# Kernel optimization log

Hardware: AMD Instinct MI355X
Metric: run time of the kernel (lower is better)

The kernel has to match this reference:

```python
import jax, jax.numpy as jnp
import numpy as np

N = 4096
IN_DIM = 128
OUT_DIM = 64
LEAKY_SLOPE = 0.2


def setup_inputs() -> dict:
    key = jax.random.key(0)
    ks = jax.random.split(key, 8)
    H = jax.random.normal(ks[0], (N, IN_DIM), dtype=jnp.float32)
    # dense 0/1 adjacency per relation (int constants w.r.t. autodiff)
    A_buys = jax.random.randint(ks[1], (N, N), 0, 2, dtype=jnp.int32)
    A_views = jax.random.randint(ks[2], (N, N), 0, 2, dtype=jnp.int32)
    # xavier_uniform for W (stored [in, out]; Wh = H @ W == torch Linear with weight W.T)
    s_w = float(np.sqrt(6.0 / (IN_DIM + OUT_DIM)))
    W_buys = jax.random.uniform(ks[3], (IN_DIM, OUT_DIM), jnp.float32, -s_w, s_w)
    W_views = jax.random.uniform(ks[4], (IN_DIM, OUT_DIM), jnp.float32, -s_w, s_w)
    # xavier_uniform on a.view(1, 2*out_dim)
    s_a = float(np.sqrt(6.0 / (1 + 2 * OUT_DIM)))
    a_buys = jax.random.uniform(ks[5], (2 * OUT_DIM,), jnp.float32, -s_a, s_a)
    a_views = jax.random.uniform(ks[6], (2 * OUT_DIM,), jnp.float32, -s_a, s_a)
    bias = jnp.zeros((OUT_DIM,), dtype=jnp.float32)
    return {"H": H, "A_buys": A_buys, "A_views": A_views,
            "W_buys": W_buys, "W_views": W_views,
            "a_buys": a_buys, "a_views": a_views, "bias": bias}


def _relation(H, A, W, a):
    Wh = H @ W                                  # [N, OUT]
    # (cat(Wh_i, Wh_j) * a).sum(-1) == Wh_i @ a[:OUT] + Wh_j @ a[OUT:]
    s_i = Wh @ a[:OUT_DIM]                      # [N]
    s_j = Wh @ a[OUT_DIM:]                      # [N]
    e = jax.nn.leaky_relu(s_i[:, None] + s_j[None, :], LEAKY_SLOPE)  # [N, N]
    e = jnp.where(A == 0, -jnp.inf, e)
    alpha = jnp.nan_to_num(jax.nn.softmax(e, axis=1))                # isolated rows -> 0
    return alpha @ Wh                           # [N, OUT]


def reference(H, A_buys, A_views, W_buys, W_views, a_buys, a_views, bias):
    agg = _relation(H, A_buys, W_buys, a_buys) + _relation(H, A_views, W_views, a_views)
    return agg + bias
```

## Files before the change

### kernel.cpp

```cpp
#include <hip/hip_runtime.h>

#define NN 4096
#define IND 128
#define OUTD 64
#define WJ 128
#define NWIN 8
#define LOG2E 1.44269504088896340736f

typedef __attribute__((ext_vector_type(4))) float  floatx4;
typedef __attribute__((ext_vector_type(8))) __bf16 bf16x8;
typedef __attribute__((ext_vector_type(4))) int    intx4;

#if __has_builtin(__builtin_amdgcn_exp2f)
#define EXP2(x) __builtin_amdgcn_exp2f(x)
#else
#define EXP2(x) exp2f(x)
#endif

__device__ __forceinline__ unsigned short f2bf(float f) {
  unsigned int u = __float_as_uint(f);
  u += 0x7fffu + ((u >> 16) & 1u);
  return (unsigned short)(u >> 16);
}

__global__ __launch_bounds__(256) void gat_prep(
    const float* __restrict__ H,
    const float* __restrict__ W0, const float* __restrict__ W1,
    const float* __restrict__ av0, const float* __restrict__ av1,
    unsigned short* __restrict__ whF,
    float* __restrict__ sA, float* __restrict__ sB)
{
  const int rel = blockIdx.y;
  const float* __restrict__ W  = rel ? W1 : W0;
  const float* __restrict__ av = rel ? av1 : av0;
  const int i0 = blockIdx.x * 16;
  const int t = threadIdx.x;
  const int c = t & 63;
  const int wv = __builtin_amdgcn_readfirstlane(t >> 6);
  const float* __restrict__ hp = H + (size_t)(i0 + wv * 4) * IND;

  float acc0 = 0.f, acc1 = 0.f, acc2 = 0.f, acc3 = 0.f;
#pragma unroll 8
  for (int k = 0; k < IND; k += 4) {
    float4 h0 = *(const float4*)(hp + k);
    float4 h1 = *(const float4*)(hp + IND + k);
    float4 h2 = *(const float4*)(hp + 2 * IND + k);
    float4 h3 = *(const float4*)(hp + 3 * IND + k);
    float w0 = W[(k + 0) * OUTD + c];
    float w1 = W[(k + 1) * OUTD + c];
    float w2 = W[(k + 2) * OUTD + c];
    float w3 = W[(k + 3) * OUTD + c];
    acc0 += h0.x * w0 + h0.y * w1 + h0.z * w2 + h0.w * w3;
    acc1 += h1.x * w0 + h1.y * w1 + h1.z * w2 + h1.w * w3;
    acc2 += h2.x * w0 + h2.y * w1 + h2.z * w2 + h2.w * w3;
    acc3 += h3.x * w0 + h3.y * w1 + h3.z * w2 + h3.w * w3;
  }

  const float alo = av[c] * LOG2E, ahi = av[OUTD + c] * LOG2E;
  float pa0 = acc0 * alo, pa1 = acc1 * alo, pa2 = acc2 * alo, pa3 = acc3 * alo;
  float pb0 = acc0 * ahi, pb1 = acc1 * ahi, pb2 = acc2 * ahi, pb3 = acc3 * ahi;
#pragma unroll
  for (int off = 32; off >= 1; off >>= 1) {
    pa0 += __shfl_xor(pa0, off); pa1 += __shfl_xor(pa1, off);
    pa2 += __shfl_xor(pa2, off); pa3 += __shfl_xor(pa3, off);
    pb0 += __shfl_xor(pb0, off); pb1 += __shfl_xor(pb1, off);
    pb2 += __shfl_xor(pb2, off); pb3 += __shfl_xor(pb3, off);
  }
  const int ibase = i0 + wv * 4;
  if (c == 0) {
    float* sa = sA + rel * NN + ibase;
    float* sb = sB + rel * NN + ibase;
    sa[0] = pa0; sa[1] = pa1; sa[2] = pa2; sa[3] = pa3;
    sb[0] = pb0; sb[1] = pb1; sb[2] = pb2; sb[3] = pb3;
  }

  unsigned long long packed =
      (unsigned long long)f2bf(acc0)        | ((unsigned long long)f2bf(acc1) << 16) |
      ((unsigned long long)f2bf(acc2) << 32) | ((unsigned long long)f2bf(acc3) << 48);
  *(unsigned long long*)(whF + ((size_t)(rel * 512 + (ibase >> 3)) * 64 + c) * 8 + (ibase & 7)) = packed;
}

__global__ __launch_bounds__(256, 2) void gat_fused(
    const int* __restrict__ A0, const int* __restrict__ A1,
    const unsigned short* __restrict__ whF,
    const float* __restrict__ sA, const float* __restrict__ sB,
    float* __restrict__ numer,
    float* __restrict__ denom)
{
  __shared__ char lds[4][2][4096];
  const int rel  = blockIdx.y;
  const int i0   = blockIdx.x * 16;
  const int t    = threadIdx.x;
  const int w    = t >> 6;
  const int lane = t & 63;
  const int quad = lane >> 4;
  const int m    = lane & 15;
  const int lj   = lane & 31;
  const int half = lane >> 5;
  const int s_st = lj >> 1;
  const int wboff = s_st * 256 + (lj & 1) * 8;
  const int* __restrict__ A = rel ? A1 : A0;
  const unsigned short* __restrict__ wh = whF + (size_t)rel * 512 * 64 * 8;
  const float* __restrict__ sbp = sB + rel * NN;

  float si_r[8];
#pragma unroll
  for (int p = 0; p < 8; p++) si_r[p] = sA[rel * NN + i0 + 2 * p + half];

  const int jbase = w * (NWIN * WJ);

  floatx4 acc0 = {0.f,0.f,0.f,0.f}, acc1 = acc0, acc2 = acc0, acc3 = acc0, acc4 = acc0;
  bf16x8 vone;
#pragma unroll
  for (int k = 0; k < 8; k++) vone[k] = (__bf16)1.0f;

  intx4  av2[2][8];
  float4 sjv2[2];
  bf16x8 b[4][4];

  auto issueA = [&](int win) {
    const int jw = jbase + win * WJ;
    const int buf = win & 1;
    sjv2[buf] = *(const float4*)(sbp + jw + lj * 4);
    const int* pA = A + (size_t)(i0 + half) * NN + jw + lj * 4;
#pragma unroll
    for (int p = 0; p < 8; p++)
      av2[buf][p] = __builtin_nontemporal_load((const intx4*)(pA + (size_t)(2 * p) * NN));
  };

  auto stage = [&](int win) {
    const int buf = win & 1;
    char* slice = lds[w][buf];
    const float4 sjv = sjv2[buf];
#pragma unroll
    for (int p = 0; p < 8; p++) {
      const int rp = 2 * p + half;
      const float si = si_r[p];
      float t0 = si + sjv.x, t1 = si + sjv.y, t2 = si + sjv.z, t3 = si + sjv.w;
      float e0 = EXP2(fmaxf(t0, 0.2f * t0));
      float e1 = EXP2(fmaxf(t1, 0.2f * t1));
      float e2 = EXP2(fmaxf(t2, 0.2f * t2));
      float e3 = EXP2(fmaxf(t3, 0.2f * t3));
      const intx4 a4 = av2[buf][p];
      e0 = a4[0] ? e0 : 0.f;
      e1 = a4[1] ? e1 : 0.f;
      e2 = a4[2] ? e2 : 0.f;
      e3 = a4[3] ? e3 : 0.f;
      uint2 pk;
      pk.x = (unsigned)f2bf(e0) | ((unsigned)f2bf(e1) << 16);
      pk.y = (unsigned)f2bf(e2) | ((unsigned)f2bf(e3) << 16);
      *(uint2*)(slice + wboff + ((rp ^ s_st) & 15) * 16) = pk;
    }
  };

  auto issueB = [&](int win) {
    const int jw = jbase + win * WJ;
    const unsigned short* bb = wh + ((size_t)(jw >> 3) + quad) * 512 + (size_t)m * 8;
#pragma unroll
    for (int ks = 0; ks < 4; ks++)
#pragma unroll
      for (int nt = 0; nt < 4; nt++)
        b[ks][nt] = *(const bf16x8*)(bb + (size_t)ks * 2048 + nt * 128);
  };

  auto domfma = [&](int win) {
    char* slice = lds[w][win & 1];
    bf16x8 afr[4];
#pragma unroll
    for (int ks = 0; ks < 4; ks++) {
      const int s = ks * 4 + quad;
      afr[ks] = *(const bf16x8*)(slice + s * 256 + ((m ^ s) & 15) * 16);
    }
#pragma unroll
    for (int ks = 0; ks < 4; ks++) {
      acc0 = __builtin_amdgcn_mfma_f32_16x16x32_bf16(afr[ks], b[ks][0], acc0, 0, 0, 0);
      acc1 = __builtin_amdgcn_mfma_f32_16x16x32_bf16(afr[ks], b[ks][1], acc1, 0, 0, 0);
      acc2 = __builtin_amdgcn_mfma_f32_16x16x32_bf16(afr[ks], b[ks][2], acc2, 0, 0, 0);
      acc3 = __builtin_amdgcn_mfma_f32_16x16x32_bf16(afr[ks], b[ks][3], acc3, 0, 0, 0);
      acc4 = __builtin_amdgcn_mfma_f32_16x16x32_bf16(afr[ks], vone,     acc4, 0, 0, 0);
    }
  };

  issueA(0);
  stage(0);
  issueA(1);

#pragma unroll
  for (int win = 0; win < NWIN; win++) {
    issueB(win);
    if (win + 2 < NWIN) issueA(win + 2);
    if (win + 1 < NWIN) stage(win + 1);
    domfma(win);
  }

  float* redw  = (float*)lds[w][0];
  float* dredw = (float*)lds[w][1];
#pragma unroll
  for (int r = 0; r < 4; r++) {
    const int row = quad * 4 + r;
    redw[row * 64 + 0 * 16 + m] = acc0[r];
    redw[row * 64 + 1 * 16 + m] = acc1[r];
    redw[row * 64 + 2 * 16 + m] = acc2[r];
    redw[row * 64 + 3 * 16 + m] = acc3[r];
  }
  if (m == 0) {
#pragma unroll
    for (int r = 0; r < 4; r++) dredw[quad * 4 + r] = acc4[r];
  }
  __syncthreads();

  const int c  = t & 63;
  const int r0 = t >> 6;
  const size_t base = (size_t)rel * NN;
#pragma unroll
  for (int rr = r0; rr < 16; rr += 4) {
    float nsum = 0.f, ds = 0.f;
#pragma unroll
    for (int ww = 0; ww < 4; ww++) {
      nsum += ((const float*)lds[ww][0])[rr * 64 + c];
      ds   += ((const float*)lds[ww][1])[rr];
    }
    numer[(base + i0 + rr) * OUTD + c] = nsum;
    if (c == 0) denom[base + i0 + rr] = ds;
  }
}

__global__ __launch_bounds__(256) void gat_combine(
    const float* __restrict__ numer, const float* __restrict__ denom,
    const float* __restrict__ bias, float* __restrict__ out)
{
  const int idx = blockIdx.x * 256 + threadIdx.x;
  const int i  = idx >> 4;
  const int c4 = idx & 15;
  const float4* nv = (const float4*)numer;

  float4 o = ((const float4*)bias)[c4];
#pragma unroll
  for (int rel = 0; rel < 2; rel++) {
    const size_t base = (size_t)rel * NN + i;
    float4 n = nv[base * 16 + c4];
    float  d = denom[base];
    float inv = d > 0.f ? 1.f / d : 0.f;
    o.x += n.x * inv; o.y += n.y * inv; o.z += n.z * inv; o.w += n.w * inv;
  }
  ((float4*)out)[idx] = o;
}

extern "C" void kernel_launch(void* const* d_in, const int* in_sizes, int n_in,
                              void* d_out, int out_size, void* d_ws, size_t ws_size,
                              hipStream_t stream) {
  const float* H    = (const float*)d_in[0];
  const int*   A0   = (const int*)d_in[1];
  const int*   A1   = (const int*)d_in[2];
  const float* W0   = (const float*)d_in[3];
  const float* W1   = (const float*)d_in[4];
  const float* av0  = (const float*)d_in[5];
  const float* av1  = (const float*)d_in[6];
  const float* bias = (const float*)d_in[7];
  float* out = (float*)d_out;

  const size_t whF_b = (size_t)2 * 512 * 64 * 8 * 2;
  const size_t s_b   = (size_t)2 * NN * 4;

  unsigned short* whF   = (unsigned short*)d_ws;
  float*          sA    = (float*)((char*)d_ws + whF_b);
  float*          sB    = (float*)((char*)d_ws + whF_b + s_b);
  float*          numer = (float*)((char*)d_ws + whF_b + 2 * s_b);
  float*          denom = numer + (size_t)2 * NN * OUTD;

  gat_prep<<<dim3(NN / 16, 2), 256, 0, stream>>>(H, W0, W1, av0, av1, whF, sA, sB);
  gat_fused<<<dim3(NN / 16, 2), 256, 0, stream>>>(A0, A1, whF, sA, sB, numer, denom);
  gat_combine<<<(NN * OUTD / 4) / 256, 256, 0, stream>>>(numer, denom, bias, out);
}
```

Before: 180.8 us.

## Fuse both relations into one block and fold the combine kernel into the epilogue

```diff
diff --git a/kernel.cpp b/kernel.cpp
--- a/kernel.cpp
+++ b/kernel.cpp
@@ -80,18 +80,18 @@
   *(unsigned long long*)(whF + ((size_t)(rel * 512 + (ibase >> 3)) * 64 + c) * 8 + (ibase & 7)) = packed;
 }
 
-__global__ __launch_bounds__(256, 2) void gat_fused(
+__global__ __launch_bounds__(512, 2) void gat_fused(
     const int* __restrict__ A0, const int* __restrict__ A1,
     const unsigned short* __restrict__ whF,
     const float* __restrict__ sA, const float* __restrict__ sB,
-    float* __restrict__ numer,
-    float* __restrict__ denom)
+    const float* __restrict__ bias,
+    float* __restrict__ out)
 {
-  __shared__ char lds[4][2][4096];
-  const int rel  = blockIdx.y;
+  __shared__ char lds[8][2][4096];
   const int i0   = blockIdx.x * 16;
   const int t    = threadIdx.x;
   const int w    = t >> 6;
+  const int rel  = w >> 2;
   const int lane = t & 63;
   const int quad = lane >> 4;
   const int m    = lane & 15;
@@ -107,7 +107,7 @@
 #pragma unroll
   for (int p = 0; p < 8; p++) si_r[p] = sA[rel * NN + i0 + 2 * p + half];
 
-  const int jbase = w * (NWIN * WJ);
+  const int jbase = (w & 3) * (NWIN * WJ);
 
   floatx4 acc0 = {0.f,0.f,0.f,0.f}, acc1 = acc0, acc2 = acc0, acc3 = acc0, acc4 = acc0;
   bf16x8 vone;
@@ -211,39 +211,21 @@
 
   const int c  = t & 63;
   const int r0 = t >> 6;
-  const size_t base = (size_t)rel * NN;
-#pragma unroll
-  for (int rr = r0; rr < 16; rr += 4) {
-    float nsum = 0.f, ds = 0.f;
+  const float bc = bias[c];
+#pragma unroll
+  for (int rr = r0; rr < 16; rr += 8) {
+    float n0 = 0.f, n1 = 0.f, d0 = 0.f, d1 = 0.f;
 #pragma unroll
     for (int ww = 0; ww < 4; ww++) {
-      nsum += ((const float*)lds[ww][0])[rr * 64 + c];
-      ds   += ((const float*)lds[ww][1])[rr];
-    }
-    numer[(base + i0 + rr) * OUTD + c] = nsum;
-    if (c == 0) denom[base + i0 + rr] = ds;
-  }
-}
-
-__global__ __launch_bounds__(256) void gat_combine(
-    const float* __restrict__ numer, const float* __restrict__ denom,
-    const float* __restrict__ bias, float* __restrict__ out)
-{
-  const int idx = blockIdx.x * 256 + threadIdx.x;
-  const int i  = idx >> 4;
-  const int c4 = idx & 15;
-  const float4* nv = (const float4*)numer;
-
-  float4 o = ((const float4*)bias)[c4];
-#pragma unroll
-  for (int rel = 0; rel < 2; rel++) {
-    const size_t base = (size_t)rel * NN + i;
-    float4 n = nv[base * 16 + c4];
-    float  d = denom[base];
-    float inv = d > 0.f ? 1.f / d : 0.f;
-    o.x += n.x * inv; o.y += n.y * inv; o.z += n.z * inv; o.w += n.w * inv;
-  }
-  ((float4*)out)[idx] = o;
+      n0 += ((const float*)lds[ww][0])[rr * 64 + c];
+      d0 += ((const float*)lds[ww][1])[rr];
+      n1 += ((const float*)lds[ww + 4][0])[rr * 64 + c];
+      d1 += ((const float*)lds[ww + 4][1])[rr];
+    }
+    const float inv0 = d0 > 0.f ? 1.f / d0 : 0.f;
+    const float inv1 = d1 > 0.f ? 1.f / d1 : 0.f;
+    out[(size_t)(i0 + rr) * OUTD + c] = n0 * inv0 + n1 * inv1 + bc;
+  }
 }
 
 extern "C" void kernel_launch(void* const* d_in, const int* in_sizes, int n_in,
@@ -262,13 +244,10 @@
   const size_t whF_b = (size_t)2 * 512 * 64 * 8 * 2;
   const size_t s_b   = (size_t)2 * NN * 4;
 
-  unsigned short* whF   = (unsigned short*)d_ws;
-  float*          sA    = (float*)((char*)d_ws + whF_b);
-  float*          sB    = (float*)((char*)d_ws + whF_b + s_b);
-  float*          numer = (float*)((char*)d_ws + whF_b + 2 * s_b);
-  float*          denom = numer + (size_t)2 * NN * OUTD;
+  unsigned short* whF = (unsigned short*)d_ws;
+  float*          sA  = (float*)((char*)d_ws + whF_b);
+  float*          sB  = (float*)((char*)d_ws + whF_b + s_b);
 
   gat_prep<<<dim3(NN / 16, 2), 256, 0, stream>>>(H, W0, W1, av0, av1, whF, sA, sB);
-  gat_fused<<<dim3(NN / 16, 2), 256, 0, stream>>>(A0, A1, whF, sA, sB, numer, denom);
-  gat_combine<<<(NN * OUTD / 4) / 256, 256, 0, stream>>>(numer, denom, bias, out);
-}
+  gat_fused<<<NN / 16, 512, 0, stream>>>(A0, A1, whF, sA, sB, bias, out);
+}
```

Measured after the change: 174.7 us (median of 2 runs). -3.4%, faster.
